# Optimization experiments

Hardware: AMD Instinct MI355X
Metric: run time of the kernel (lower is better)

## Reference

```python
import jax, jax.numpy as jnp
import numpy as np

B, LT, LS, D, H = 2, 2048, 2048, 1024, 16
HD = D // H  # head_dim = 64


def setup_inputs() -> dict:
    key = jax.random.key(0)
    ks = jax.random.split(key, 7)
    s = 1.0 / np.sqrt(D)
    return {
        "x": jax.random.normal(ks[0], (B, LT, D), jnp.float32),
        "memory": jax.random.normal(ks[1], (B, LS, D), jnp.float32),
        "position_embedding": jax.random.normal(ks[2], (1, H, LT, LS), jnp.float32) * 0.02,
        "mask": jnp.zeros((LT, LS), jnp.float32),
        "Wq": jax.random.normal(ks[3], (D, D), jnp.float32) * s,
        "Wk": jax.random.normal(ks[4], (D, D), jnp.float32) * s,
        "Wv": jax.random.normal(ks[5], (D, D), jnp.float32) * s,
        "Wo": jax.random.normal(ks[6], (D, D), jnp.float32) * s,
    }


def reference(x, memory, position_embedding, mask, Wq, Wk, Wv, Wo):
    b, lt, _ = x.shape
    ls = memory.shape[1]
    # q/k/v projections (bias-free Linear), split into heads: [B,H,L,HD]
    q = (x @ Wq).reshape(b, lt, H, HD).transpose(0, 2, 1, 3)
    k = (memory @ Wk).reshape(b, ls, H, HD).transpose(0, 2, 1, 3)
    v = (memory @ Wv).reshape(b, ls, H, HD).transpose(0, 2, 1, 3)
    # scaled QK^T + position bias + additive mask
    attn = jnp.einsum("bhtd,bhsd->bhts", q, k) / jnp.sqrt(jnp.float32(HD))
    attn = attn + position_embedding
    attn = attn + mask.reshape(1, 1, lt, ls)
    score = jnp.einsum("bhts,bhsd->bhtd", jax.nn.softmax(attn, axis=-1), v)
    score_cat = score.transpose(0, 2, 1, 3).reshape(b, lt, D)
    score_proj = score_cat @ Wo
    return score_proj, k, v
```

## Files before the change

kernel.cpp:

```cpp
#include <hip/hip_runtime.h>
#include <hip/hip_bf16.h>
#include <stdint.h>

#define NB 2
#define NH 16
#define LT 2048
#define LS 2048
#define DIM 1024
#define HD 64

typedef __attribute__((ext_vector_type(4))) float f32x4;
typedef __attribute__((ext_vector_type(8))) short short8;
typedef __attribute__((ext_vector_type(4))) short short4v;

__device__ __forceinline__ short f2bf(float f) {
  __hip_bfloat16 h = __float2bfloat16(f);
  return *reinterpret_cast<short*>(&h);
}

__device__ __forceinline__ void gl_lds16(const short* g, short* l) {
  __builtin_amdgcn_global_load_lds((const __attribute__((address_space(1))) void*)g,
                                   (__attribute__((address_space(3))) void*)l, 16, 0, 0);
}

__global__ __launch_bounds__(256) void prep_kernel(const float* __restrict__ x, const float* __restrict__ memory,
                                                   const float* __restrict__ Wq, const float* __restrict__ Wk,
                                                   const float* __restrict__ Wv, const float* __restrict__ Wo,
                                                   short* __restrict__ wt, short* __restrict__ xbf,
                                                   short* __restrict__ membf) {
  __shared__ float tile[64][68];
  const int bid = blockIdx.x;
  const int tid = threadIdx.x;
  if (bid < 1024) {
    const int widx = bid >> 8;
    const int rem = bid & 255;
    const int kt = rem >> 4, nt = rem & 15;
    const float* W = (widx == 0) ? Wq : (widx == 1) ? Wk : (widx == 2) ? Wv : Wo;
    {
      const int r = tid >> 2, c0 = (tid & 3) << 4;
      const float* src = W + (size_t)(kt * 64 + r) * DIM + nt * 64 + c0;
#pragma unroll
      for (int j = 0; j < 4; ++j)
        *reinterpret_cast<f32x4*>(&tile[r][c0 + 4 * j]) = *reinterpret_cast<const f32x4*>(src + 4 * j);
    }
    __syncthreads();
    {
      const int n = tid >> 2, k0 = (tid & 3) << 4;
      short outv[16];
#pragma unroll
      for (int j = 0; j < 16; ++j) outv[j] = f2bf(tile[k0 + j][n]);
      short* dst = wt + (size_t)widx * DIM * DIM + (size_t)(nt * 64 + n) * DIM + kt * 64 + k0;
      *reinterpret_cast<short8*>(dst) = *reinterpret_cast<short8*>(&outv[0]);
      *reinterpret_cast<short8*>(dst + 8) = *reinterpret_cast<short8*>(&outv[8]);
    }
  } else {
    const int cid = bid - 1024;
    const float* src = (cid < 1024) ? x : memory;
    short* dst = (cid < 1024) ? xbf : membf;
    const size_t base = (size_t)(cid & 1023) * 4096 + (size_t)tid * 16;
    const float* s = src + base;
    const f32x4 f0 = *reinterpret_cast<const f32x4*>(s);
    const f32x4 f1 = *reinterpret_cast<const f32x4*>(s + 4);
    const f32x4 f2 = *reinterpret_cast<const f32x4*>(s + 8);
    const f32x4 f3 = *reinterpret_cast<const f32x4*>(s + 12);
    short8 o0, o1;
#pragma unroll
    for (int j = 0; j < 4; ++j) {
      o0[j] = f2bf(f0[j]);
      o0[4 + j] = f2bf(f1[j]);
      o1[j] = f2bf(f2[j]);
      o1[4 + j] = f2bf(f3[j]);
    }
    *reinterpret_cast<short8*>(dst + base) = o0;
    *reinterpret_cast<short8*>(dst + base + 8) = o1;
  }
}

template <int TM, int MF>
__device__ __forceinline__ void mm_loop(const short* __restrict__ A, const short* __restrict__ Bt, short* a_lds,
                                        short* b_lds, int bm, int bn, int w, int lane, f32x4 (&acc)[MF][4]) {
  const int lm = lane & 15, g = lane >> 4;
  const int wr = w >> 1, wc = w & 1;
  const int lr8 = lane >> 3;
  const int gch = (lane & 7) ^ (lr8 & 7);
  const short* Aw = A + (size_t)(bm * TM + w * 8 + lr8) * 1024 + gch * 8;
  const short* Bw = Bt + (size_t)(bn * 128 + w * 8 + lr8) * 1024 + gch * 8;
  short* al = a_lds + w * 512;
  short* bl = b_lds + w * 512;
  const int axor = lm & 7;
  constexpr int JA = TM / 32;

  for (int k0 = 0; k0 < 1024; k0 += 64) {
    __syncthreads();
#pragma unroll
    for (int j = 0; j < JA; ++j) gl_lds16(Aw + (size_t)j * 32 * 1024 + k0, al + j * 2048);
#pragma unroll
    for (int j = 0; j < 4; ++j) gl_lds16(Bw + (size_t)j * 32 * 1024 + k0, bl + j * 2048);
    __syncthreads();
    short8 afr[MF][2], bfr[4][2];
#pragma unroll
    for (int mi = 0; mi < MF; ++mi)
#pragma unroll
      for (int kk = 0; kk < 2; ++kk)
        afr[mi][kk] = *reinterpret_cast<const short8*>(
            &a_lds[(wr * (TM / 2) + mi * 16 + lm) * 64 + (((kk << 2) + g) ^ axor) * 8]);
#pragma unroll
    for (int nj = 0; nj < 4; ++nj)
#pragma unroll
      for (int kk = 0; kk < 2; ++kk)
        bfr[nj][kk] = *reinterpret_cast<const short8*>(
            &b_lds[(wc * 64 + nj * 16 + lm) * 64 + (((kk << 2) + g) ^ axor) * 8]);
#pragma unroll
    for (int mi = 0; mi < MF; ++mi)
#pragma unroll
      for (int nj = 0; nj < 4; ++nj)
#pragma unroll
        for (int kk = 0; kk < 2; ++kk)
          acc[mi][nj] = __builtin_amdgcn_mfma_f32_16x16x32_bf16(afr[mi][kk], bfr[nj][kk], acc[mi][nj], 0, 0, 0);
  }
}

__global__ __launch_bounds__(256, 3) void qkv_gemm(const short* __restrict__ xbf, const short* __restrict__ membf,
                                                   const short* __restrict__ wt, short* __restrict__ q_ws,
                                                   float* __restrict__ k_out, short* __restrict__ k_bf,
                                                   float* __restrict__ v_out, short* __restrict__ v_bf) {
  __shared__ short a_lds[128 * 64];
  __shared__ short b_lds[128 * 64];
  const int bid = blockIdx.x;
  const int seg = bid >> 8, rem = bid & 255;
  const int bm = rem & 31, bn = rem >> 5;
  const int tid = threadIdx.x, lane = tid & 63, w = tid >> 6;
  const short* A = (seg == 0) ? xbf : membf;
  const short* B = wt + ((size_t)seg << 20);
  f32x4 acc[4][4];
#pragma unroll
  for (int i = 0; i < 4; ++i)
#pragma unroll
    for (int j = 0; j < 4; ++j) acc[i][j] = (f32x4){0.f, 0.f, 0.f, 0.f};
  mm_loop<128, 4>(A, B, a_lds, b_lds, bm, bn, w, lane, acc);

  const int lm = lane & 15, g4 = (lane >> 4) << 2;
  const int wr = w >> 1, wc = w & 1;
#pragma unroll
  for (int mi = 0; mi < 4; ++mi)
#pragma unroll
    for (int nj = 0; nj < 4; ++nj)
#pragma unroll
      for (int r = 0; r < 4; ++r) {
        const int row = bm * 128 + wr * 64 + mi * 16 + g4 + r;
        const int col = bn * 128 + wc * 64 + nj * 16 + lm;
        const float v = acc[mi][nj][r];
        const int b = row >> 11, t = row & 2047, hh = col >> 6, hd = col & 63;
        const size_t idx = (((size_t)b * NH + hh) * LS + t) * HD + hd;
        if (seg == 0) {
          q_ws[idx] = f2bf(v);
        } else if (seg == 1) {
          k_out[idx] = v;
          k_bf[idx] = f2bf(v);
        } else {
          v_out[idx] = v;
          v_bf[idx] = f2bf(v);
        }
      }
}

__global__ __launch_bounds__(256, 3) void o_gemm(const short* __restrict__ attn_bf, const short* __restrict__ wto,
                                                 float* __restrict__ outp) {
  __shared__ short a_lds[64 * 64];
  __shared__ short b_lds[128 * 64];
  const int bid = blockIdx.x;
  const int bm = bid & 63, bn = bid >> 6;
  const int tid = threadIdx.x, lane = tid & 63, w = tid >> 6;
  f32x4 acc[2][4];
#pragma unroll
  for (int i = 0; i < 2; ++i)
#pragma unroll
    for (int j = 0; j < 4; ++j) acc[i][j] = (f32x4){0.f, 0.f, 0.f, 0.f};
  mm_loop<64, 2>(attn_bf, wto, a_lds, b_lds, bm, bn, w, lane, acc);

  const int lm = lane & 15, g4 = (lane >> 4) << 2;
  const int wr = w >> 1, wc = w & 1;
#pragma unroll
  for (int mi = 0; mi < 2; ++mi)
#pragma unroll
    for (int nj = 0; nj < 4; ++nj)
#pragma unroll
      for (int r = 0; r < 4; ++r) {
        const int row = bm * 64 + wr * 32 + mi * 16 + g4 + r;
        const int col = bn * 128 + wc * 64 + nj * 16 + lm;
        outp[(size_t)row * DIM + col] = acc[mi][nj][r];
      }
}

__global__ __launch_bounds__(256, 4) void attn_kernel(const short* __restrict__ qw, const short* __restrict__ kbf,
                                                      const short* __restrict__ vbf, const float* __restrict__ pe,
                                                      const float* __restrict__ mask, short* __restrict__ aout) {
  __shared__ short k_lds[64][72];
  __shared__ short vt_lds[64][72];
  __shared__ short p_lds[4][16][72];
  __shared__ float sc_lds[4][16];
  __shared__ float l_lds[4][16];
  const int bid = blockIdx.x;
  const int b = bid & 1;
  const int qt = (bid >> 1) & 31;
  const int h = (bid >> 6) & 15;
  const int bh = b * NH + h;
  const int tid = threadIdx.x, lane = tid & 63, w = tid >> 6;
  const int qbase = qt * 64 + w * 16;
  const int lm = lane & 15, g = lane >> 4, g8 = g << 3, g4 = g << 2;
  constexpr float L2E = 1.4426950408889634f;

  typedef __attribute__((ext_vector_type(2))) short short2v;

  short8 qfr[2];
#pragma unroll
  for (int kk = 0; kk < 2; ++kk)
    qfr[kk] = *reinterpret_cast<const short8*>(qw + ((size_t)bh * LT + qbase + lm) * HD + kk * 32 + g8);

  float m_run = -1e30f, l_run = 0.f;
  f32x4 acc_o[4];
#pragma unroll
  for (int dj = 0; dj < 4; ++dj) acc_o[dj] = (f32x4){0.f, 0.f, 0.f, 0.f};

  const int t_lane = qbase + lm;
  const float* pe_row = pe + (size_t)h * LT * LS + (size_t)t_lane * LS;
  const float* mask_row = mask + (size_t)t_lane * LS;

  const int srow = tid >> 2, scol0 = (tid & 3) << 4;
  const int vs2 = (lane & 31) << 1;
  const int vd0 = (w << 4) + ((lane >> 5) << 3);

  for (int s0 = 0; s0 < LS; s0 += 64) {
    {
      const short* ksrc = kbf + ((size_t)bh * LS + s0 + srow) * HD + scol0;
      *reinterpret_cast<short8*>(&k_lds[srow][scol0]) = *reinterpret_cast<const short8*>(ksrc);
      *reinterpret_cast<short8*>(&k_lds[srow][scol0 + 8]) = *reinterpret_cast<const short8*>(ksrc + 8);
    }
    {
      const short* vsrc = vbf + ((size_t)bh * LS + s0 + vs2) * HD + vd0;
      const short8 va = *reinterpret_cast<const short8*>(vsrc);
      const short8 vb = *reinterpret_cast<const short8*>(vsrc + HD);
#pragma unroll
      for (int j = 0; j < 8; ++j) {
        short2v pr = {va[j], vb[j]};
        *reinterpret_cast<short2v*>(&vt_lds[vd0 + j][vs2]) = pr;
      }
    }
    __syncthreads();

    f32x4 pv4[4], mv4[4];
#pragma unroll
    for (int nj = 0; nj < 4; ++nj) {
      const int sbase = s0 + nj * 16 + g4;
      pv4[nj] = *reinterpret_cast<const f32x4*>(pe_row + sbase);
      mv4[nj] = *reinterpret_cast<const f32x4*>(mask_row + sbase);
    }

    f32x4 accs[4];
#pragma unroll
    for (int nj = 0; nj < 4; ++nj) {
      accs[nj] = (f32x4){0.f, 0.f, 0.f, 0.f};
#pragma unroll
      for (int kk = 0; kk < 2; ++kk) {
        const short8 kfr = *reinterpret_cast<const short8*>(&k_lds[nj * 16 + lm][kk * 32 + g8]);
        accs[nj] = __builtin_amdgcn_mfma_f32_16x16x32_bf16(kfr, qfr[kk], accs[nj], 0, 0, 0);
      }
    }

#pragma unroll
    for (int nj = 0; nj < 4; ++nj)
#pragma unroll
      for (int r = 0; r < 4; ++r) accs[nj][r] = fmaf(accs[nj][r], 0.125f, pv4[nj][r] + mv4[nj][r]);

    float mx = accs[0][0];
#pragma unroll
    for (int nj = 0; nj < 4; ++nj)
#pragma unroll
      for (int r = 0; r < 4; ++r) mx = fmaxf(mx, accs[nj][r]);
    mx = fmaxf(mx, __shfl_xor(mx, 16));
    mx = fmaxf(mx, __shfl_xor(mx, 32));
    const float mnew = fmaxf(m_run, mx);
    const float nm = mnew * L2E;
    float rs = 0.f;
#pragma unroll
    for (int nj = 0; nj < 4; ++nj)
#pragma unroll
      for (int r = 0; r < 4; ++r) {
        const float p = exp2f(fmaf(accs[nj][r], L2E, -nm));
        accs[nj][r] = p;
        rs += p;
      }
    rs += __shfl_xor(rs, 16);
    rs += __shfl_xor(rs, 32);
    const float sc = exp2f(fmaf(m_run, L2E, -nm));
    l_run = l_run * sc + rs;
    m_run = mnew;

#pragma unroll
    for (int nj = 0; nj < 4; ++nj) {
      short4v pk = {f2bf(accs[nj][0]), f2bf(accs[nj][1]), f2bf(accs[nj][2]), f2bf(accs[nj][3])};
      *reinterpret_cast<short4v*>(&p_lds[w][lm][nj * 16 + g4]) = pk;
    }
    if (g == 0) sc_lds[w][lm] = sc;
    const f32x4 sc4 = *reinterpret_cast<const f32x4*>(&sc_lds[w][g4]);
#pragma unroll
    for (int dj = 0; dj < 4; ++dj)
#pragma unroll
      for (int r = 0; r < 4; ++r) acc_o[dj][r] *= sc4[r];

#pragma unroll
    for (int kk = 0; kk < 2; ++kk) {
      const short8 pfr = *reinterpret_cast<const short8*>(&p_lds[w][lm][kk * 32 + g8]);
#pragma unroll
      for (int dj = 0; dj < 4; ++dj) {
        const short8 vfr = *reinterpret_cast<const short8*>(&vt_lds[dj * 16 + lm][kk * 32 + g8]);
        acc_o[dj] = __builtin_amdgcn_mfma_f32_16x16x32_bf16(pfr, vfr, acc_o[dj], 0, 0, 0);
      }
    }
    __syncthreads();
  }

  if (g == 0) l_lds[w][lm] = l_run;
  const f32x4 l4 = *reinterpret_cast<const f32x4*>(&l_lds[w][g4]);
#pragma unroll
  for (int r = 0; r < 4; ++r) {
    const float inv = 1.f / l4[r];
    const int t = qbase + g4 + r;
#pragma unroll
    for (int dj = 0; dj < 4; ++dj) {
      const int d = dj * 16 + lm;
      aout[((size_t)b * LT + t) * DIM + h * HD + d] = f2bf(acc_o[dj][r] * inv);
    }
  }
}

extern "C" void kernel_launch(void* const* d_in, const int* in_sizes, int n_in, void* d_out, int out_size,
                              void* d_ws, size_t ws_size, hipStream_t stream) {
  (void)in_sizes;
  (void)n_in;
  (void)out_size;
  (void)ws_size;
  const float* x = (const float*)d_in[0];
  const float* memory = (const float*)d_in[1];
  const float* pe = (const float*)d_in[2];
  const float* mask = (const float*)d_in[3];
  const float* Wq = (const float*)d_in[4];
  const float* Wk = (const float*)d_in[5];
  const float* Wv = (const float*)d_in[6];
  const float* Wo = (const float*)d_in[7];
  float* outp = (float*)d_out;
  float* k_out = outp + (size_t)NB * NH * LS * HD;
  float* v_out = k_out + (size_t)NB * NH * LS * HD;
  char* ws = (char*)d_ws;
  short* q_ws = (short*)ws;
  short* attn_ws = (short*)(ws + (8u << 20));
  short* wt = (short*)(ws + (16u << 20));
  short* k_bf = (short*)(ws + (24u << 20));
  short* v_bf = (short*)(ws + (32u << 20));
  short* xbf = (short*)(ws + (40u << 20));
  short* membf = (short*)(ws + (48u << 20));

  prep_kernel<<<dim3(3072), dim3(256), 0, stream>>>(x, memory, Wq, Wk, Wv, Wo, wt, xbf, membf);
  qkv_gemm<<<dim3(768), dim3(256), 0, stream>>>(xbf, membf, wt, q_ws, k_out, k_bf, v_out, v_bf);
  attn_kernel<<<dim3(1024), dim3(256), 0, stream>>>(q_ws, k_bf, v_bf, pe, mask, attn_ws);
  o_gemm<<<dim3(512), dim3(256), 0, stream>>>(attn_ws, wt + (3u << 20), outp);
}
```

Before: 253.3 us.

## Process both batches per attention block to share position-embedding loads; swizzle LDS

Each attention block now handles both batch elements for one head and query tile, so every position-embedding and mask value read from global memory is used twice rather than loaded separately by two blocks. This halves the traffic on the large fp32 bias tensor, at the cost of doubling the per-block register state and halving the grid size. LDS tiles move from padded arrays to XOR-swizzled layouts to avoid bank conflicts. Shared-memory round trips for the rescale and normalizer values are replaced by lane shuffles.

```diff
diff --git a/kernel.cpp b/kernel.cpp
--- a/kernel.cpp
+++ b/kernel.cpp
@@ -12,11 +12,14 @@
 typedef __attribute__((ext_vector_type(4))) float f32x4;
 typedef __attribute__((ext_vector_type(8))) short short8;
 typedef __attribute__((ext_vector_type(4))) short short4v;
+typedef __attribute__((ext_vector_type(2))) short short2v;
 
 __device__ __forceinline__ short f2bf(float f) {
   __hip_bfloat16 h = __float2bfloat16(f);
   return *reinterpret_cast<short*>(&h);
 }
+
+__device__ __forceinline__ int swz(int row, int bc) { return (row << 7) + (bc ^ ((row & 7) << 4)); }
 
 __device__ __forceinline__ void gl_lds16(const short* g, short* l) {
   __builtin_amdgcn_global_load_lds((const __attribute__((address_space(1))) void*)g,
@@ -195,141 +198,154 @@
 __global__ __launch_bounds__(256, 4) void attn_kernel(const short* __restrict__ qw, const short* __restrict__ kbf,
                                                       const short* __restrict__ vbf, const float* __restrict__ pe,
                                                       const float* __restrict__ mask, short* __restrict__ aout) {
-  __shared__ short k_lds[64][72];
-  __shared__ short vt_lds[64][72];
-  __shared__ short p_lds[4][16][72];
-  __shared__ float sc_lds[4][16];
-  __shared__ float l_lds[4][16];
+  __shared__ __align__(16) char k_raw[2][8192];
+  __shared__ __align__(16) char vt_raw[2][8192];
+  __shared__ __align__(16) char p_raw[8192];
   const int bid = blockIdx.x;
-  const int b = bid & 1;
-  const int qt = (bid >> 1) & 31;
-  const int h = (bid >> 6) & 15;
-  const int bh = b * NH + h;
+  const int qt = bid & 31;
+  const int h = bid >> 5;
   const int tid = threadIdx.x, lane = tid & 63, w = tid >> 6;
   const int qbase = qt * 64 + w * 16;
-  const int lm = lane & 15, g = lane >> 4, g8 = g << 3, g4 = g << 2;
+  const int lm = lane & 15, g = lane >> 4, g8 = g << 3, g16 = g << 4, g4 = g << 2;
   constexpr float L2E = 1.4426950408889634f;
 
-  typedef __attribute__((ext_vector_type(2))) short short2v;
-
-  short8 qfr[2];
-#pragma unroll
-  for (int kk = 0; kk < 2; ++kk)
-    qfr[kk] = *reinterpret_cast<const short8*>(qw + ((size_t)bh * LT + qbase + lm) * HD + kk * 32 + g8);
-
-  float m_run = -1e30f, l_run = 0.f;
-  f32x4 acc_o[4];
-#pragma unroll
-  for (int dj = 0; dj < 4; ++dj) acc_o[dj] = (f32x4){0.f, 0.f, 0.f, 0.f};
+  short8 qfr[2][2];
+#pragma unroll
+  for (int bb = 0; bb < 2; ++bb)
+#pragma unroll
+    for (int kk = 0; kk < 2; ++kk)
+      qfr[bb][kk] = *reinterpret_cast<const short8*>(qw + ((size_t)(bb * NH + h) * LT + qbase + lm) * HD +
+                                                     kk * 32 + g8);
+
+  float m_run[2] = {-1e30f, -1e30f}, l_run[2] = {0.f, 0.f};
+  f32x4 acc_o[2][4];
+#pragma unroll
+  for (int bb = 0; bb < 2; ++bb)
+#pragma unroll
+    for (int dj = 0; dj < 4; ++dj) acc_o[bb][dj] = (f32x4){0.f, 0.f, 0.f, 0.f};
 
   const int t_lane = qbase + lm;
   const float* pe_row = pe + (size_t)h * LT * LS + (size_t)t_lane * LS;
   const float* mask_row = mask + (size_t)t_lane * LS;
 
   const int srow = tid >> 2, scol0 = (tid & 3) << 4;
+  const int kb = scol0 * 2;
   const int vs2 = (lane & 31) << 1;
   const int vd0 = (w << 4) + ((lane >> 5) << 3);
 
   for (int s0 = 0; s0 < LS; s0 += 64) {
-    {
-      const short* ksrc = kbf + ((size_t)bh * LS + s0 + srow) * HD + scol0;
-      *reinterpret_cast<short8*>(&k_lds[srow][scol0]) = *reinterpret_cast<const short8*>(ksrc);
-      *reinterpret_cast<short8*>(&k_lds[srow][scol0 + 8]) = *reinterpret_cast<const short8*>(ksrc + 8);
-    }
-    {
-      const short* vsrc = vbf + ((size_t)bh * LS + s0 + vs2) * HD + vd0;
+#pragma unroll
+    for (int bb = 0; bb < 2; ++bb) {
+      const size_t bh = (size_t)(bb * NH + h);
+      const short* ksrc = kbf + (bh * LS + s0 + srow) * HD + scol0;
+      *reinterpret_cast<short8*>(k_raw[bb] + swz(srow, kb)) = *reinterpret_cast<const short8*>(ksrc);
+      *reinterpret_cast<short8*>(k_raw[bb] + swz(srow, kb + 16)) = *reinterpret_cast<const short8*>(ksrc + 8);
+      const short* vsrc = vbf + (bh * LS + s0 + vs2) * HD + vd0;
       const short8 va = *reinterpret_cast<const short8*>(vsrc);
       const short8 vb = *reinterpret_cast<const short8*>(vsrc + HD);
 #pragma unroll
       for (int j = 0; j < 8; ++j) {
         short2v pr = {va[j], vb[j]};
-        *reinterpret_cast<short2v*>(&vt_lds[vd0 + j][vs2]) = pr;
-      }
-    }
-    __syncthreads();
-
-    f32x4 pv4[4], mv4[4];
-#pragma unroll
-    for (int nj = 0; nj < 4; ++nj) {
-      const int sbase = s0 + nj * 16 + g4;
-      pv4[nj] = *reinterpret_cast<const f32x4*>(pe_row + sbase);
-      mv4[nj] = *reinterpret_cast<const f32x4*>(mask_row + sbase);
-    }
-
-    f32x4 accs[4];
-#pragma unroll
-    for (int nj = 0; nj < 4; ++nj) {
-      accs[nj] = (f32x4){0.f, 0.f, 0.f, 0.f};
+        *reinterpret_cast<short2v*>(vt_raw[bb] + swz(vd0 + j, vs2 * 2)) = pr;
+      }
+    }
+    __syncthreads();
+
+    f32x4 pm[4];
+    {
+      f32x4 mv[4];
+#pragma unroll
+      for (int nj = 0; nj < 4; ++nj) {
+        const int sb = s0 + nj * 16 + g4;
+        pm[nj] = *reinterpret_cast<const f32x4*>(pe_row + sb);
+        mv[nj] = *reinterpret_cast<const f32x4*>(mask_row + sb);
+      }
+#pragma unroll
+      for (int nj = 0; nj < 4; ++nj) pm[nj] += mv[nj];
+    }
+
+#pragma unroll
+    for (int bb = 0; bb < 2; ++bb) {
+      f32x4 accs[4];
+#pragma unroll
+      for (int nj = 0; nj < 4; ++nj) {
+        accs[nj] = (f32x4){0.f, 0.f, 0.f, 0.f};
+#pragma unroll
+        for (int kk = 0; kk < 2; ++kk) {
+          const short8 kfr = *reinterpret_cast<const short8*>(k_raw[bb] + swz(nj * 16 + lm, kk * 64 + g16));
+          accs[nj] = __builtin_amdgcn_mfma_f32_16x16x32_bf16(kfr, qfr[bb][kk], accs[nj], 0, 0, 0);
+        }
+      }
+
+#pragma unroll
+      for (int nj = 0; nj < 4; ++nj)
+#pragma unroll
+        for (int r = 0; r < 4; ++r) accs[nj][r] = fmaf(accs[nj][r], 0.125f, pm[nj][r]);
+
+      float mx = accs[0][0];
+#pragma unroll
+      for (int nj = 0; nj < 4; ++nj)
+#pragma unroll
+        for (int r = 0; r < 4; ++r) mx = fmaxf(mx, accs[nj][r]);
+      mx = fmaxf(mx, __shfl_xor(mx, 16));
+      mx = fmaxf(mx, __shfl_xor(mx, 32));
+      const float mnew = fmaxf(m_run[bb], mx);
+      const float nm = mnew * L2E;
+      float rs = 0.f;
+#pragma unroll
+      for (int nj = 0; nj < 4; ++nj)
+#pragma unroll
+        for (int r = 0; r < 4; ++r) {
+          const float p = exp2f(fmaf(accs[nj][r], L2E, -nm));
+          accs[nj][r] = p;
+          rs += p;
+        }
+      rs += __shfl_xor(rs, 16);
+      rs += __shfl_xor(rs, 32);
+      const float sc = exp2f(fmaf(m_run[bb], L2E, -nm));
+      l_run[bb] = l_run[bb] * sc + rs;
+      m_run[bb] = mnew;
+
+#pragma unroll
+      for (int nj = 0; nj < 4; ++nj) {
+        short4v pk = {f2bf(accs[nj][0]), f2bf(accs[nj][1]), f2bf(accs[nj][2]), f2bf(accs[nj][3])};
+        *reinterpret_cast<short4v*>(p_raw + (w << 11) + swz(lm, nj * 32 + g * 8)) = pk;
+      }
+      float sc4[4];
+#pragma unroll
+      for (int r = 0; r < 4; ++r) sc4[r] = __shfl(sc, g4 + r);
+#pragma unroll
+      for (int dj = 0; dj < 4; ++dj)
+#pragma unroll
+        for (int r = 0; r < 4; ++r) acc_o[bb][dj][r] *= sc4[r];
+
 #pragma unroll
       for (int kk = 0; kk < 2; ++kk) {
-        const short8 kfr = *reinterpret_cast<const short8*>(&k_lds[nj * 16 + lm][kk * 32 + g8]);
-        accs[nj] = __builtin_amdgcn_mfma_f32_16x16x32_bf16(kfr, qfr[kk], accs[nj], 0, 0, 0);
-      }
-    }
-
-#pragma unroll
-    for (int nj = 0; nj < 4; ++nj)
-#pragma unroll
-      for (int r = 0; r < 4; ++r) accs[nj][r] = fmaf(accs[nj][r], 0.125f, pv4[nj][r] + mv4[nj][r]);
-
-    float mx = accs[0][0];
-#pragma unroll
-    for (int nj = 0; nj < 4; ++nj)
-#pragma unroll
-      for (int r = 0; r < 4; ++r) mx = fmaxf(mx, accs[nj][r]);
-    mx = fmaxf(mx, __shfl_xor(mx, 16));
-    mx = fmaxf(mx, __shfl_xor(mx, 32));
-    const float mnew = fmaxf(m_run, mx);
-    const float nm = mnew * L2E;
-    float rs = 0.f;
-#pragma unroll
-    for (int nj = 0; nj < 4; ++nj)
-#pragma unroll
-      for (int r = 0; r < 4; ++r) {
-        const float p = exp2f(fmaf(accs[nj][r], L2E, -nm));
-        accs[nj][r] = p;
-        rs += p;
-      }
-    rs += __shfl_xor(rs, 16);
-    rs += __shfl_xor(rs, 32);
-    const float sc = exp2f(fmaf(m_run, L2E, -nm));
-    l_run = l_run * sc + rs;
-    m_run = mnew;
-
-#pragma unroll
-    for (int nj = 0; nj < 4; ++nj) {
-      short4v pk = {f2bf(accs[nj][0]), f2bf(accs[nj][1]), f2bf(accs[nj][2]), f2bf(accs[nj][3])};
-      *reinterpret_cast<short4v*>(&p_lds[w][lm][nj * 16 + g4]) = pk;
-    }
-    if (g == 0) sc_lds[w][lm] = sc;
-    const f32x4 sc4 = *reinterpret_cast<const f32x4*>(&sc_lds[w][g4]);
-#pragma unroll
-    for (int dj = 0; dj < 4; ++dj)
-#pragma unroll
-      for (int r = 0; r < 4; ++r) acc_o[dj][r] *= sc4[r];
-
-#pragma unroll
-    for (int kk = 0; kk < 2; ++kk) {
-      const short8 pfr = *reinterpret_cast<const short8*>(&p_lds[w][lm][kk * 32 + g8]);
+        const short8 pfr = *reinterpret_cast<const short8*>(p_raw + (w << 11) + swz(lm, kk * 64 + g16));
+#pragma unroll
+        for (int dj = 0; dj < 4; ++dj) {
+          const short8 vfr = *reinterpret_cast<const short8*>(vt_raw[bb] + swz(dj * 16 + lm, kk * 64 + g16));
+          acc_o[bb][dj] = __builtin_amdgcn_mfma_f32_16x16x32_bf16(pfr, vfr, acc_o[bb][dj], 0, 0, 0);
+        }
+      }
+    }
+    __syncthreads();
+  }
+
+#pragma unroll
+  for (int bb = 0; bb < 2; ++bb) {
+    float l4[4];
+#pragma unroll
+    for (int r = 0; r < 4; ++r) l4[r] = __shfl(l_run[bb], g4 + r);
+#pragma unroll
+    for (int r = 0; r < 4; ++r) {
+      const float inv = 1.f / l4[r];
+      const int t = qbase + g4 + r;
 #pragma unroll
       for (int dj = 0; dj < 4; ++dj) {
-        const short8 vfr = *reinterpret_cast<const short8*>(&vt_lds[dj * 16 + lm][kk * 32 + g8]);
-        acc_o[dj] = __builtin_amdgcn_mfma_f32_16x16x32_bf16(pfr, vfr, acc_o[dj], 0, 0, 0);
-      }
-    }
-    __syncthreads();
-  }
-
-  if (g == 0) l_lds[w][lm] = l_run;
-  const f32x4 l4 = *reinterpret_cast<const f32x4*>(&l_lds[w][g4]);
-#pragma unroll
-  for (int r = 0; r < 4; ++r) {
-    const float inv = 1.f / l4[r];
-    const int t = qbase + g4 + r;
-#pragma unroll
-    for (int dj = 0; dj < 4; ++dj) {
-      const int d = dj * 16 + lm;
-      aout[((size_t)b * LT + t) * DIM + h * HD + d] = f2bf(acc_o[dj][r] * inv);
+        const int d = dj * 16 + lm;
+        aout[((size_t)bb * LT + t) * DIM + h * HD + d] = f2bf(acc_o[bb][dj][r] * inv);
+      }
     }
   }
 }
@@ -362,6 +378,6 @@
 
   prep_kernel<<<dim3(3072), dim3(256), 0, stream>>>(x, memory, Wq, Wk, Wv, Wo, wt, xbf, membf);
   qkv_gemm<<<dim3(768), dim3(256), 0, stream>>>(xbf, membf, wt, q_ws, k_out, k_bf, v_out, v_bf);
-  attn_kernel<<<dim3(1024), dim3(256), 0, stream>>>(q_ws, k_bf, v_bf, pe, mask, attn_ws);
+  attn_kernel<<<dim3(512), dim3(256), 0, stream>>>(q_ws, k_bf, v_bf, pe, mask, attn_ws);
   o_gemm<<<dim3(512), dim3(256), 0, stream>>>(attn_ws, wt + (3u << 20), outp);
 }
```

Measured after the change: 391.9 us. 54.7% more time.

## Double-buffer V tile, load K fragments from global, fold softmax scale into Q

Applied to the files above, without the earlier changes.

The attention kernel now loads K fragments straight from global memory into registers instead of staging them through LDS. It double-buffers the transposed V tile so the next tile's global loads overlap the current compute, with one barrier per iteration. The 1/sqrt(d) scale is folded into Q when it is written to bf16, which removes a multiply per score. In exchange, each wave redundantly fetches K from global (relying on cache hits), register pressure rises, and LDS use for V doubles.

```diff
diff --git a/kernel.cpp b/kernel.cpp
--- a/kernel.cpp
+++ b/kernel.cpp
@@ -12,6 +12,7 @@
 typedef __attribute__((ext_vector_type(4))) float f32x4;
 typedef __attribute__((ext_vector_type(8))) short short8;
 typedef __attribute__((ext_vector_type(4))) short short4v;
+typedef __attribute__((ext_vector_type(2))) short short2v;
 
 __device__ __forceinline__ short f2bf(float f) {
   __hip_bfloat16 h = __float2bfloat16(f);
@@ -153,7 +154,7 @@
         const int b = row >> 11, t = row & 2047, hh = col >> 6, hd = col & 63;
         const size_t idx = (((size_t)b * NH + hh) * LS + t) * HD + hd;
         if (seg == 0) {
-          q_ws[idx] = f2bf(v);
+          q_ws[idx] = f2bf(v * 0.125f);
         } else if (seg == 1) {
           k_out[idx] = v;
           k_bf[idx] = f2bf(v);
@@ -195,8 +196,7 @@
 __global__ __launch_bounds__(256, 4) void attn_kernel(const short* __restrict__ qw, const short* __restrict__ kbf,
                                                       const short* __restrict__ vbf, const float* __restrict__ pe,
                                                       const float* __restrict__ mask, short* __restrict__ aout) {
-  __shared__ short k_lds[64][72];
-  __shared__ short vt_lds[64][72];
+  __shared__ short vt_lds[2][64][72];
   __shared__ short p_lds[4][16][72];
   __shared__ float sc_lds[4][16];
   __shared__ float l_lds[4][16];
@@ -210,8 +210,6 @@
   const int lm = lane & 15, g = lane >> 4, g8 = g << 3, g4 = g << 2;
   constexpr float L2E = 1.4426950408889634f;
 
-  typedef __attribute__((ext_vector_type(2))) short short2v;
-
   short8 qfr[2];
 #pragma unroll
   for (int kk = 0; kk < 2; ++kk)
@@ -226,51 +224,66 @@
   const float* pe_row = pe + (size_t)h * LT * LS + (size_t)t_lane * LS;
   const float* mask_row = mask + (size_t)t_lane * LS;
 
-  const int srow = tid >> 2, scol0 = (tid & 3) << 4;
+  const short* k_base = kbf + ((size_t)bh * LS + lm) * HD + g8;
+
   const int vs2 = (lane & 31) << 1;
   const int vd0 = (w << 4) + ((lane >> 5) << 3);
+  const short* v_base = vbf + ((size_t)bh * LS + vs2) * HD + vd0;
+
+#define V_WRITE(BUF, VA, VB)                                            \
+  _Pragma("unroll") for (int j = 0; j < 8; ++j) {                       \
+    short2v pr = {VA[j], VB[j]};                                        \
+    *reinterpret_cast<short2v*>(&vt_lds[BUF][vd0 + j][vs2]) = pr;       \
+  }
+
+  {
+    const short8 va = *reinterpret_cast<const short8*>(v_base);
+    const short8 vb = *reinterpret_cast<const short8*>(v_base + HD);
+    V_WRITE(0, va, vb)
+  }
+  __syncthreads();
 
   for (int s0 = 0; s0 < LS; s0 += 64) {
+    const int buf = (s0 >> 6) & 1;
+    short8 vnA, vnB;
+    const bool have_next = (s0 + 64 < LS);
+    if (have_next) {
+      const short* vn = v_base + (size_t)(s0 + 64) * HD;
+      vnA = *reinterpret_cast<const short8*>(vn);
+      vnB = *reinterpret_cast<const short8*>(vn + HD);
+    }
+    f32x4 pm[4];
     {
-      const short* ksrc = kbf + ((size_t)bh * LS + s0 + srow) * HD + scol0;
-      *reinterpret_cast<short8*>(&k_lds[srow][scol0]) = *reinterpret_cast<const short8*>(ksrc);
-      *reinterpret_cast<short8*>(&k_lds[srow][scol0 + 8]) = *reinterpret_cast<const short8*>(ksrc + 8);
-    }
-    {
-      const short* vsrc = vbf + ((size_t)bh * LS + s0 + vs2) * HD + vd0;
-      const short8 va = *reinterpret_cast<const short8*>(vsrc);
-      const short8 vb = *reinterpret_cast<const short8*>(vsrc + HD);
-#pragma unroll
-      for (int j = 0; j < 8; ++j) {
-        short2v pr = {va[j], vb[j]};
-        *reinterpret_cast<short2v*>(&vt_lds[vd0 + j][vs2]) = pr;
-      }
-    }
-    __syncthreads();
-
-    f32x4 pv4[4], mv4[4];
-#pragma unroll
-    for (int nj = 0; nj < 4; ++nj) {
-      const int sbase = s0 + nj * 16 + g4;
-      pv4[nj] = *reinterpret_cast<const f32x4*>(pe_row + sbase);
-      mv4[nj] = *reinterpret_cast<const f32x4*>(mask_row + sbase);
-    }
+      f32x4 mv[4];
+#pragma unroll
+      for (int nj = 0; nj < 4; ++nj) {
+        const int sb = s0 + nj * 16 + g4;
+        pm[nj] = *reinterpret_cast<const f32x4*>(pe_row + sb);
+        mv[nj] = *reinterpret_cast<const f32x4*>(mask_row + sb);
+      }
+#pragma unroll
+      for (int nj = 0; nj < 4; ++nj) pm[nj] += mv[nj];
+    }
+    short8 kfr[4][2];
+#pragma unroll
+    for (int nj = 0; nj < 4; ++nj)
+#pragma unroll
+      for (int kk = 0; kk < 2; ++kk)
+        kfr[nj][kk] = *reinterpret_cast<const short8*>(k_base + (size_t)(s0 + nj * 16) * HD + kk * 32);
 
     f32x4 accs[4];
 #pragma unroll
     for (int nj = 0; nj < 4; ++nj) {
       accs[nj] = (f32x4){0.f, 0.f, 0.f, 0.f};
 #pragma unroll
-      for (int kk = 0; kk < 2; ++kk) {
-        const short8 kfr = *reinterpret_cast<const short8*>(&k_lds[nj * 16 + lm][kk * 32 + g8]);
-        accs[nj] = __builtin_amdgcn_mfma_f32_16x16x32_bf16(kfr, qfr[kk], accs[nj], 0, 0, 0);
-      }
-    }
-
-#pragma unroll
-    for (int nj = 0; nj < 4; ++nj)
-#pragma unroll
-      for (int r = 0; r < 4; ++r) accs[nj][r] = fmaf(accs[nj][r], 0.125f, pv4[nj][r] + mv4[nj][r]);
+      for (int kk = 0; kk < 2; ++kk)
+        accs[nj] = __builtin_amdgcn_mfma_f32_16x16x32_bf16(kfr[nj][kk], qfr[kk], accs[nj], 0, 0, 0);
+    }
+
+#pragma unroll
+    for (int nj = 0; nj < 4; ++nj)
+#pragma unroll
+      for (int r = 0; r < 4; ++r) accs[nj][r] += pm[nj][r];
 
     float mx = accs[0][0];
 #pragma unroll
@@ -313,12 +326,15 @@
       const short8 pfr = *reinterpret_cast<const short8*>(&p_lds[w][lm][kk * 32 + g8]);
 #pragma unroll
       for (int dj = 0; dj < 4; ++dj) {
-        const short8 vfr = *reinterpret_cast<const short8*>(&vt_lds[dj * 16 + lm][kk * 32 + g8]);
+        const short8 vfr = *reinterpret_cast<const short8*>(&vt_lds[buf][dj * 16 + lm][kk * 32 + g8]);
         acc_o[dj] = __builtin_amdgcn_mfma_f32_16x16x32_bf16(pfr, vfr, acc_o[dj], 0, 0, 0);
       }
     }
+
+    if (have_next) V_WRITE(buf ^ 1, vnA, vnB)
     __syncthreads();
   }
+#undef V_WRITE
 
   if (g == 0) l_lds[w][lm] = l_run;
   const f32x4 l4 = *reinterpret_cast<const f32x4*>(&l_lds[w][g4]);
```

Measured after the change: 350.4 us. 38.3% more time.

## Split attention over two key halves with an LSE combine kernel and swizzled LDS

Applied to the files above, without the earlier changes.

Each (batch, head, query tile) attention block now processes only half of the key/value sequence, which doubles the grid. Per-half partial outputs and log-sum-exp values go to workspace, and a new combine kernel merges them into the bf16 attention output. LDS tiles switch to an XOR-swizzled layout to cut bank conflicts, the 1/sqrt(d) scale is folded into Q at projection time, and the occupancy hint rises to 6. The split costs an extra kernel launch, an extra round trip of partial outputs through memory, and some precision because the partials are stored in bf16.

```diff
diff --git a/kernel.cpp b/kernel.cpp
--- a/kernel.cpp
+++ b/kernel.cpp
@@ -12,11 +12,20 @@
 typedef __attribute__((ext_vector_type(4))) float f32x4;
 typedef __attribute__((ext_vector_type(8))) short short8;
 typedef __attribute__((ext_vector_type(4))) short short4v;
+typedef __attribute__((ext_vector_type(2))) short short2v;
 
 __device__ __forceinline__ short f2bf(float f) {
   __hip_bfloat16 h = __float2bfloat16(f);
   return *reinterpret_cast<short*>(&h);
 }
+
+__device__ __forceinline__ float b2f(short s) {
+  union { unsigned u; float f; } v;
+  v.u = ((unsigned)(unsigned short)s) << 16;
+  return v.f;
+}
+
+__device__ __forceinline__ int swz(int row, int bc) { return (row << 7) + (bc ^ ((row & 7) << 4)); }
 
 __device__ __forceinline__ void gl_lds16(const short* g, short* l) {
   __builtin_amdgcn_global_load_lds((const __attribute__((address_space(1))) void*)g,
@@ -153,7 +162,7 @@
         const int b = row >> 11, t = row & 2047, hh = col >> 6, hd = col & 63;
         const size_t idx = (((size_t)b * NH + hh) * LS + t) * HD + hd;
         if (seg == 0) {
-          q_ws[idx] = f2bf(v);
+          q_ws[idx] = f2bf(v * 0.125f);
         } else if (seg == 1) {
           k_out[idx] = v;
           k_bf[idx] = f2bf(v);
@@ -192,25 +201,25 @@
       }
 }
 
-__global__ __launch_bounds__(256, 4) void attn_kernel(const short* __restrict__ qw, const short* __restrict__ kbf,
+__global__ __launch_bounds__(256, 6) void attn_kernel(const short* __restrict__ qw, const short* __restrict__ kbf,
                                                       const short* __restrict__ vbf, const float* __restrict__ pe,
-                                                      const float* __restrict__ mask, short* __restrict__ aout) {
-  __shared__ short k_lds[64][72];
-  __shared__ short vt_lds[64][72];
-  __shared__ short p_lds[4][16][72];
+                                                      const float* __restrict__ mask, short* __restrict__ pO,
+                                                      float* __restrict__ lse_ws) {
+  __shared__ __align__(16) char k_raw[8192];
+  __shared__ __align__(16) char vt_raw[8192];
+  __shared__ __align__(16) char p_raw[8192];
   __shared__ float sc_lds[4][16];
   __shared__ float l_lds[4][16];
   const int bid = blockIdx.x;
   const int b = bid & 1;
   const int qt = (bid >> 1) & 31;
   const int h = (bid >> 6) & 15;
+  const int sh = bid >> 10;
   const int bh = b * NH + h;
   const int tid = threadIdx.x, lane = tid & 63, w = tid >> 6;
   const int qbase = qt * 64 + w * 16;
-  const int lm = lane & 15, g = lane >> 4, g8 = g << 3, g4 = g << 2;
+  const int lm = lane & 15, g = lane >> 4, g8 = g << 3, g16 = g << 4, g4 = g << 2;
   constexpr float L2E = 1.4426950408889634f;
-
-  typedef __attribute__((ext_vector_type(2))) short short2v;
 
   short8 qfr[2];
 #pragma unroll
@@ -227,33 +236,39 @@
   const float* mask_row = mask + (size_t)t_lane * LS;
 
   const int srow = tid >> 2, scol0 = (tid & 3) << 4;
+  const int kb = scol0 * 2;
   const int vs2 = (lane & 31) << 1;
   const int vd0 = (w << 4) + ((lane >> 5) << 3);
 
-  for (int s0 = 0; s0 < LS; s0 += 64) {
+  const int s_beg = sh * (LS / 2), s_end = s_beg + (LS / 2);
+
+  for (int s0 = s_beg; s0 < s_end; s0 += 64) {
     {
       const short* ksrc = kbf + ((size_t)bh * LS + s0 + srow) * HD + scol0;
-      *reinterpret_cast<short8*>(&k_lds[srow][scol0]) = *reinterpret_cast<const short8*>(ksrc);
-      *reinterpret_cast<short8*>(&k_lds[srow][scol0 + 8]) = *reinterpret_cast<const short8*>(ksrc + 8);
-    }
-    {
+      *reinterpret_cast<short8*>(k_raw + swz(srow, kb)) = *reinterpret_cast<const short8*>(ksrc);
+      *reinterpret_cast<short8*>(k_raw + swz(srow, kb + 16)) = *reinterpret_cast<const short8*>(ksrc + 8);
       const short* vsrc = vbf + ((size_t)bh * LS + s0 + vs2) * HD + vd0;
       const short8 va = *reinterpret_cast<const short8*>(vsrc);
       const short8 vb = *reinterpret_cast<const short8*>(vsrc + HD);
 #pragma unroll
       for (int j = 0; j < 8; ++j) {
         short2v pr = {va[j], vb[j]};
-        *reinterpret_cast<short2v*>(&vt_lds[vd0 + j][vs2]) = pr;
+        *reinterpret_cast<short2v*>(vt_raw + swz(vd0 + j, vs2 * 2)) = pr;
       }
     }
     __syncthreads();
 
-    f32x4 pv4[4], mv4[4];
-#pragma unroll
-    for (int nj = 0; nj < 4; ++nj) {
-      const int sbase = s0 + nj * 16 + g4;
-      pv4[nj] = *reinterpret_cast<const f32x4*>(pe_row + sbase);
-      mv4[nj] = *reinterpret_cast<const f32x4*>(mask_row + sbase);
+    f32x4 pm[4];
+    {
+      f32x4 mv[4];
+#pragma unroll
+      for (int nj = 0; nj < 4; ++nj) {
+        const int sb = s0 + nj * 16 + g4;
+        pm[nj] = *reinterpret_cast<const f32x4*>(pe_row + sb);
+        mv[nj] = *reinterpret_cast<const f32x4*>(mask_row + sb);
+      }
+#pragma unroll
+      for (int nj = 0; nj < 4; ++nj) pm[nj] += mv[nj];
     }
 
     f32x4 accs[4];
@@ -262,7 +277,7 @@
       accs[nj] = (f32x4){0.f, 0.f, 0.f, 0.f};
 #pragma unroll
       for (int kk = 0; kk < 2; ++kk) {
-        const short8 kfr = *reinterpret_cast<const short8*>(&k_lds[nj * 16 + lm][kk * 32 + g8]);
+        const short8 kfr = *reinterpret_cast<const short8*>(k_raw + swz(nj * 16 + lm, kk * 64 + g16));
         accs[nj] = __builtin_amdgcn_mfma_f32_16x16x32_bf16(kfr, qfr[kk], accs[nj], 0, 0, 0);
       }
     }
@@ -270,7 +285,7 @@
 #pragma unroll
     for (int nj = 0; nj < 4; ++nj)
 #pragma unroll
-      for (int r = 0; r < 4; ++r) accs[nj][r] = fmaf(accs[nj][r], 0.125f, pv4[nj][r] + mv4[nj][r]);
+      for (int r = 0; r < 4; ++r) accs[nj][r] += pm[nj][r];
 
     float mx = accs[0][0];
 #pragma unroll
@@ -299,7 +314,7 @@
 #pragma unroll
     for (int nj = 0; nj < 4; ++nj) {
       short4v pk = {f2bf(accs[nj][0]), f2bf(accs[nj][1]), f2bf(accs[nj][2]), f2bf(accs[nj][3])};
-      *reinterpret_cast<short4v*>(&p_lds[w][lm][nj * 16 + g4]) = pk;
+      *reinterpret_cast<short4v*>(p_raw + (w << 11) + swz(lm, nj * 32 + g * 8)) = pk;
     }
     if (g == 0) sc_lds[w][lm] = sc;
     const f32x4 sc4 = *reinterpret_cast<const f32x4*>(&sc_lds[w][g4]);
@@ -310,10 +325,10 @@
 
 #pragma unroll
     for (int kk = 0; kk < 2; ++kk) {
-      const short8 pfr = *reinterpret_cast<const short8*>(&p_lds[w][lm][kk * 32 + g8]);
+      const short8 pfr = *reinterpret_cast<const short8*>(p_raw + (w << 11) + swz(lm, kk * 64 + g16));
 #pragma unroll
       for (int dj = 0; dj < 4; ++dj) {
-        const short8 vfr = *reinterpret_cast<const short8*>(&vt_lds[dj * 16 + lm][kk * 32 + g8]);
+        const short8 vfr = *reinterpret_cast<const short8*>(vt_raw + swz(dj * 16 + lm, kk * 64 + g16));
         acc_o[dj] = __builtin_amdgcn_mfma_f32_16x16x32_bf16(pfr, vfr, acc_o[dj], 0, 0, 0);
       }
     }
@@ -321,17 +336,44 @@
   }
 
   if (g == 0) l_lds[w][lm] = l_run;
+  if (g == 0) lse_ws[((size_t)(sh * NB + b) * NH + h) * LT + t_lane] = fmaf(m_run, L2E, __log2f(l_run));
   const f32x4 l4 = *reinterpret_cast<const f32x4*>(&l_lds[w][g4]);
 #pragma unroll
   for (int r = 0; r < 4; ++r) {
     const float inv = 1.f / l4[r];
     const int t = qbase + g4 + r;
+    const size_t prow = ((size_t)(sh * NB + b) * NH + h) * LT + t;
 #pragma unroll
     for (int dj = 0; dj < 4; ++dj) {
       const int d = dj * 16 + lm;
-      aout[((size_t)b * LT + t) * DIM + h * HD + d] = f2bf(acc_o[dj][r] * inv);
+      pO[prow * HD + d] = f2bf(acc_o[dj][r] * inv);
     }
   }
+}
+
+__global__ __launch_bounds__(256) void combine_kernel(const short* __restrict__ pO,
+                                                      const float* __restrict__ lse,
+                                                      short* __restrict__ aout) {
+  const int gid = blockIdx.x * 256 + threadIdx.x;
+  const int row = gid >> 3;
+  const int d0 = (gid & 7) << 3;
+  const int b = row >> 15;
+  const int h = (row >> 11) & 15;
+  const int t = row & 2047;
+  const size_t r0 = (size_t)row;
+  const size_t r1 = (size_t)row + (size_t)NB * NH * LT;
+  const float l0 = lse[r0], l1 = lse[r1];
+  const float mm = fmaxf(l0, l1);
+  float w0 = exp2f(l0 - mm), w1 = exp2f(l1 - mm);
+  const float inv = 1.f / (w0 + w1);
+  w0 *= inv;
+  w1 *= inv;
+  const short8 o0 = *reinterpret_cast<const short8*>(pO + r0 * HD + d0);
+  const short8 o1 = *reinterpret_cast<const short8*>(pO + r1 * HD + d0);
+  short8 out;
+#pragma unroll
+  for (int j = 0; j < 8; ++j) out[j] = f2bf(b2f(o0[j]) * w0 + b2f(o1[j]) * w1);
+  *reinterpret_cast<short8*>(aout + ((size_t)b * LT + t) * DIM + h * HD + d0) = out;
 }
 
 extern "C" void kernel_launch(void* const* d_in, const int* in_sizes, int n_in, void* d_out, int out_size,
@@ -359,9 +401,13 @@
   short* v_bf = (short*)(ws + (32u << 20));
   short* xbf = (short*)(ws + (40u << 20));
   short* membf = (short*)(ws + (48u << 20));
+  short* pO = xbf;
+  float* lse_ws = (float*)(ws + (16u << 20) + (6u << 20));
+  lse_ws = (float*)(ws + (16u << 20));
 
   prep_kernel<<<dim3(3072), dim3(256), 0, stream>>>(x, memory, Wq, Wk, Wv, Wo, wt, xbf, membf);
   qkv_gemm<<<dim3(768), dim3(256), 0, stream>>>(xbf, membf, wt, q_ws, k_out, k_bf, v_out, v_bf);
-  attn_kernel<<<dim3(1024), dim3(256), 0, stream>>>(q_ws, k_bf, v_bf, pe, mask, attn_ws);
+  attn_kernel<<<dim3(2048), dim3(256), 0, stream>>>(q_ws, k_bf, v_bf, pe, mask, pO, lse_ws);
+  combine_kernel<<<dim3(2048), dim3(256), 0, stream>>>(pO, lse_ws, attn_ws);
   o_gemm<<<dim3(512), dim3(256), 0, stream>>>(attn_ws, wt + (3u << 20), outp);
 }
```

New measurement: 378.1 us. +49.3%, slower.
